# Optimization experiments

Measured on AMD Instinct MI355X. Metric: run time of the kernel, lower is better.

Reference implementation:

```python
import jax, jax.numpy as jnp
import numpy as np

LAMBDA_L = 0.01
LAMBDA_S = 0.01
EPS = 1e-8
N_ADMIN = 512


def setup_inputs() -> dict:
    key = jax.random.key(0)
    k1, k2, k3, k4 = jax.random.split(key, 4)
    B, H, W = 8, 1024, 1024
    lights = jax.random.uniform(k1, (B, 1, H, W), dtype=jnp.float32)
    settlement = jax.random.uniform(k2, (B, 1, H, W), dtype=jnp.float32)
    admin_ids = jax.random.randint(k3, (B, H, W), 0, N_ADMIN, dtype=jnp.int32)
    # census population totals per admin unit (all ids present)
    census_totals = jax.random.uniform(k4, (N_ADMIN,), dtype=jnp.float32) * 1e5 + 1.0
    return {"lights": lights, "settlement": settlement,
            "admin_ids": admin_ids, "census_totals": census_totals}


def reference(lights, settlement, admin_ids, census_totals):
    # score = (lights + lam_L) * (settlement + lam_S), shape (B,1,H,W)
    score = (lights + LAMBDA_L) * (settlement + LAMBDA_S)
    B, _, H, W = score.shape
    n_admin = census_totals.shape[0]
    # per-batch segment ids offset so the segment-sum is a single fused reduce
    seg = admin_ids + n_admin * jnp.arange(B, dtype=admin_ids.dtype)[:, None, None]
    sums = jax.ops.segment_sum(score[:, 0].reshape(-1), seg.reshape(-1),
                               num_segments=B * n_admin)  # (B*n_admin,)
    sums = sums.reshape(B, n_admin) + EPS  # S_A + eps per (batch, admin)
    factor = census_totals[None, :] / sums  # C_A / S_A, shape (B, n_admin)
    b_idx = jnp.arange(B)[:, None, None]
    baseline = score[:, 0] * factor[b_idx, admin_ids]  # gather per pixel
    return baseline[:, None]  # (B,1,H,W)
```

## Files before the change

kernel.cpp:

```cpp
#include <hip/hip_runtime.h>

#define BATCH   8
#define HW      (1024 * 1024)
#define NA      512
#define EPSV    1e-8f
#define LAML    0.01f
#define LAMS    0.01f

#define BPB      128
#define NBLOCKS  (BATCH * BPB)
#define PIXB     (HW / BPB)
#define UNROLL   8

#define NCOPY    16
#define SCALE    4194304.0f
#define INVSCALE (1.0f / 4194304.0f)

__global__ __launch_bounds__(256, 4) void k_sums(const float* __restrict__ lights,
                                                 const float* __restrict__ settle,
                                                 const int*   __restrict__ admin,
                                                 float*       __restrict__ partial,
                                                 unsigned*    __restrict__ pck) {
    __shared__ unsigned int bins[NA * NCOPY];
    const int tid = threadIdx.x;

    #pragma unroll
    for (int i = tid; i < NA * NCOPY; i += 256) bins[i] = 0u;
    __syncthreads();

    const long base = (long)blockIdx.x * PIXB;

    const float4* __restrict__ L4 = (const float4*)(lights + base);
    const float4* __restrict__ S4 = (const float4*)(settle + base);
    const int4*   __restrict__ A4 = (const int4*)(admin + base);
    uint4*        __restrict__ P4 = (uint4*)(pck + base);

    float4 l[UNROLL], s[UNROLL];
    int4   a[UNROLL];
    #pragma unroll
    for (int u = 0; u < UNROLL; ++u) {
        const int v = tid + u * 256;
        l[u] = L4[v];
        s[u] = S4[v];
        a[u] = A4[v];
    }
    __builtin_amdgcn_sched_barrier(0);

    const int c = tid & (NCOPY - 1);
    #pragma unroll
    for (int u = 0; u < UNROLL; ++u) {
        const unsigned qx = (unsigned)((l[u].x + LAML) * (s[u].x + LAMS) * SCALE + 0.5f);
        const unsigned qy = (unsigned)((l[u].y + LAML) * (s[u].y + LAMS) * SCALE + 0.5f);
        const unsigned qz = (unsigned)((l[u].z + LAML) * (s[u].z + LAMS) * SCALE + 0.5f);
        const unsigned qw = (unsigned)((l[u].w + LAML) * (s[u].w + LAMS) * SCALE + 0.5f);
        uint4 pk;
        pk.x = ((unsigned)a[u].x << 23) | qx;
        pk.y = ((unsigned)a[u].y << 23) | qy;
        pk.z = ((unsigned)a[u].z << 23) | qz;
        pk.w = ((unsigned)a[u].w << 23) | qw;
        P4[tid + u * 256] = pk;
        atomicAdd(&bins[a[u].x * NCOPY + c], qx);
        atomicAdd(&bins[a[u].y * NCOPY + c], qy);
        atomicAdd(&bins[a[u].z * NCOPY + c], qz);
        atomicAdd(&bins[a[u].w * NCOPY + c], qw);
    }
    __syncthreads();

    float* dst = partial + (long)blockIdx.x * NA;
    for (int i = tid; i < NA; i += 256) {
        unsigned long long t = 0;
        #pragma unroll
        for (int k = 0; k < NCOPY; ++k) t += bins[i * NCOPY + k];
        dst[i] = (float)t * INVSCALE;
    }
}

__global__ __launch_bounds__(256) void k_reduce(const float* __restrict__ partial,
                                                const float* __restrict__ census,
                                                float*       __restrict__ factor) {
    __shared__ float red[256];
    const int b     = blockIdx.x >> 3;
    const int slice = blockIdx.x & 7;
    const int lane  = threadIdx.x & 63;
    const int g     = threadIdx.x >> 6;
    const int a     = slice * 64 + lane;

    const float* p = partial + (long)b * BPB * NA + a;
    float acc = 0.0f;
    #pragma unroll 8
    for (int cc = g * 32; cc < g * 32 + 32; ++cc) acc += p[(long)cc * NA];
    red[threadIdx.x] = acc;
    __syncthreads();
    if (threadIdx.x < 128) red[threadIdx.x] += red[threadIdx.x + 128];
    __syncthreads();
    if (threadIdx.x < 64) {
        float t = red[threadIdx.x] + red[threadIdx.x + 64];
        factor[b * NA + a] = census[a] / (t + EPSV);
    }
}

__global__ __launch_bounds__(256, 4) void k_out(const unsigned* __restrict__ pck,
                                                const float*    __restrict__ factor,
                                                float*          __restrict__ out) {
    __shared__ float lfac[NA];
    const int tid = threadIdx.x;
    const int b   = blockIdx.x >> 7;

    for (int i = tid; i < NA; i += 256)
        lfac[i] = factor[b * NA + i];
    __syncthreads();

    const long base = (long)blockIdx.x * PIXB;
    const uint4* __restrict__ P4 = (const uint4*)(pck + base);
    float4*      __restrict__ O4 = (float4*)(out + base);

    uint4 p[UNROLL];
    #pragma unroll
    for (int u = 0; u < UNROLL; ++u) p[u] = P4[tid + u * 256];
    __builtin_amdgcn_sched_barrier(0);

    #pragma unroll
    for (int u = 0; u < UNROLL; ++u) {
        float4 o;
        o.x = (float)(p[u].x & 0x7FFFFFu) * INVSCALE * lfac[p[u].x >> 23];
        o.y = (float)(p[u].y & 0x7FFFFFu) * INVSCALE * lfac[p[u].y >> 23];
        o.z = (float)(p[u].z & 0x7FFFFFu) * INVSCALE * lfac[p[u].z >> 23];
        o.w = (float)(p[u].w & 0x7FFFFFu) * INVSCALE * lfac[p[u].w >> 23];
        O4[tid + u * 256] = o;
    }
}

extern "C" void kernel_launch(void* const* d_in, const int* in_sizes, int n_in,
                              void* d_out, int out_size, void* d_ws, size_t ws_size,
                              hipStream_t stream) {
    const float* lights = (const float*)d_in[0];
    const float* settle = (const float*)d_in[1];
    const int*   admin  = (const int*)d_in[2];
    const float* census = (const float*)d_in[3];
    float*       out    = (float*)d_out;

    float* partial = (float*)d_ws;
    float* factor  = (float*)d_ws + (long)NBLOCKS * NA;
    unsigned* pck  = (unsigned*)d_out;

    k_sums  <<<NBLOCKS, 256, 0, stream>>>(lights, settle, admin, partial, pck);
    k_reduce<<<64,      256, 0, stream>>>(partial, census, factor);
    k_out   <<<NBLOCKS, 256, 0, stream>>>(pck, factor, out);
}
```

Measured before the change: 41.85 us.

## Fuse per-batch reduction into histogram kernel via global atomics and last-block finalize

Removes the separate k_reduce kernel. Each histogram block now atomically adds its per-admin integer sums into a global u64 array, and the last block per batch (found via an atomic counter) computes the census factors. A memset is added to zero the accumulators and counters, which adds a launch and global atomic traffic. The output kernel also switches to nontemporal stores.

```diff
diff --git a/kernel.cpp b/kernel.cpp
--- a/kernel.cpp
+++ b/kernel.cpp
@@ -16,20 +16,30 @@
 #define SCALE    4194304.0f
 #define INVSCALE (1.0f / 4194304.0f)
 
-__global__ __launch_bounds__(256, 4) void k_sums(const float* __restrict__ lights,
-                                                 const float* __restrict__ settle,
-                                                 const int*   __restrict__ admin,
-                                                 float*       __restrict__ partial,
-                                                 unsigned*    __restrict__ pck) {
+#define PAD      64
+
+typedef unsigned long long u64;
+typedef float vf4 __attribute__((ext_vector_type(4)));
+
+__global__ __launch_bounds__(256, 4)
+void k_sums(const float* __restrict__ lights,
+            const float* __restrict__ settle,
+            const int*   __restrict__ admin,
+            const float* __restrict__ census,
+            u64*         __restrict__ gsum,
+            unsigned*    __restrict__ ctr,
+            float*       __restrict__ factor,
+            unsigned*    __restrict__ pck) {
     __shared__ unsigned int bins[NA * NCOPY];
+    __shared__ unsigned int last;
     const int tid = threadIdx.x;
+    const int b   = blockIdx.x >> 7;
 
     #pragma unroll
     for (int i = tid; i < NA * NCOPY; i += 256) bins[i] = 0u;
     __syncthreads();
 
     const long base = (long)blockIdx.x * PIXB;
-
     const float4* __restrict__ L4 = (const float4*)(lights + base);
     const float4* __restrict__ S4 = (const float4*)(settle + base);
     const int4*   __restrict__ A4 = (const int4*)(admin + base);
@@ -66,36 +76,27 @@
     }
     __syncthreads();
 
-    float* dst = partial + (long)blockIdx.x * NA;
     for (int i = tid; i < NA; i += 256) {
-        unsigned long long t = 0;
+        u64 t = 0;
         #pragma unroll
         for (int k = 0; k < NCOPY; ++k) t += bins[i * NCOPY + k];
-        dst[i] = (float)t * INVSCALE;
+        atomicAdd(&gsum[b * NA + i], t);
     }
-}
+    __syncthreads();
 
-__global__ __launch_bounds__(256) void k_reduce(const float* __restrict__ partial,
-                                                const float* __restrict__ census,
-                                                float*       __restrict__ factor) {
-    __shared__ float red[256];
-    const int b     = blockIdx.x >> 3;
-    const int slice = blockIdx.x & 7;
-    const int lane  = threadIdx.x & 63;
-    const int g     = threadIdx.x >> 6;
-    const int a     = slice * 64 + lane;
-
-    const float* p = partial + (long)b * BPB * NA + a;
-    float acc = 0.0f;
-    #pragma unroll 8
-    for (int cc = g * 32; cc < g * 32 + 32; ++cc) acc += p[(long)cc * NA];
-    red[threadIdx.x] = acc;
+    if (tid == 0) {
+        unsigned prev = __hip_atomic_fetch_add(&ctr[b * PAD], 1u,
+                                               __ATOMIC_ACQ_REL,
+                                               __HIP_MEMORY_SCOPE_AGENT);
+        last = (prev == (unsigned)(BPB - 1)) ? 1u : 0u;
+    }
     __syncthreads();
-    if (threadIdx.x < 128) red[threadIdx.x] += red[threadIdx.x + 128];
-    __syncthreads();
-    if (threadIdx.x < 64) {
-        float t = red[threadIdx.x] + red[threadIdx.x + 64];
-        factor[b * NA + a] = census[a] / (t + EPSV);
+    if (last) {
+        for (int i = tid; i < NA; i += 256) {
+            u64 t = __hip_atomic_load(&gsum[b * NA + i], __ATOMIC_RELAXED,
+                                      __HIP_MEMORY_SCOPE_AGENT);
+            factor[b * NA + i] = census[i] / ((float)t * INVSCALE + EPSV);
+        }
     }
 }
 
@@ -112,7 +113,7 @@
 
     const long base = (long)blockIdx.x * PIXB;
     const uint4* __restrict__ P4 = (const uint4*)(pck + base);
-    float4*      __restrict__ O4 = (float4*)(out + base);
+    vf4*         __restrict__ O4 = (vf4*)(out + base);
 
     uint4 p[UNROLL];
     #pragma unroll
@@ -121,12 +122,12 @@
 
     #pragma unroll
     for (int u = 0; u < UNROLL; ++u) {
-        float4 o;
+        vf4 o;
         o.x = (float)(p[u].x & 0x7FFFFFu) * INVSCALE * lfac[p[u].x >> 23];
         o.y = (float)(p[u].y & 0x7FFFFFu) * INVSCALE * lfac[p[u].y >> 23];
         o.z = (float)(p[u].z & 0x7FFFFFu) * INVSCALE * lfac[p[u].z >> 23];
         o.w = (float)(p[u].w & 0x7FFFFFu) * INVSCALE * lfac[p[u].w >> 23];
-        O4[tid + u * 256] = o;
+        __builtin_nontemporal_store(o, &O4[tid + u * 256]);
     }
 }
 
@@ -139,11 +140,16 @@
     const float* census = (const float*)d_in[3];
     float*       out    = (float*)d_out;
 
-    float* partial = (float*)d_ws;
-    float* factor  = (float*)d_ws + (long)NBLOCKS * NA;
-    unsigned* pck  = (unsigned*)d_out;
+    u64*      gsum   = (u64*)d_ws;
+    unsigned* ctr    = (unsigned*)((char*)d_ws + BATCH * NA * sizeof(u64));
+    float*    factor = (float*)(ctr + BATCH * PAD);
+    unsigned* pck    = (unsigned*)d_out;
 
-    k_sums  <<<NBLOCKS, 256, 0, stream>>>(lights, settle, admin, partial, pck);
-    k_reduce<<<64,      256, 0, stream>>>(partial, census, factor);
-    k_out   <<<NBLOCKS, 256, 0, stream>>>(pck, factor, out);
+    (void)hipMemsetAsync(d_ws, 0,
+                         BATCH * NA * sizeof(u64) + BATCH * PAD * sizeof(unsigned),
+                         stream);
+
+    k_sums<<<NBLOCKS, 256, 0, stream>>>(lights, settle, admin, census,
+                                        gsum, ctr, factor, pck);
+    k_out <<<NBLOCKS, 256, 0, stream>>>(pck, factor, out);
 }
```

New measurement: 73.32 us. 1.75x slower.
